# Kernel tuning notes

Hardware: AMD Instinct MI355X
Metric: run time of the kernel (lower is better)

Reference implementation:

```python
import jax, jax.numpy as jnp
import numpy as np

B, C, T = 32, 32, 1024
K = 64          # kernel_size
DIL = 1         # dilation
MLP_DIM = 256
HID = 256       # mlp_hidden_dim; TanhBlock dims: 256 -> 256 -> 128 -> 1
NF = min(MLP_DIM, K // 2 + 1)          # 33 rfft bins kept
FFT_DIM = C * NF * 2                   # 2112
N_WIN = T - DIL * (K - 1)              # 961 windows


def setup_inputs() -> dict:
    key = jax.random.key(0)
    ks = jax.random.split(key, 8)
    s = 0.02
    return {
        "x": jax.random.normal(ks[0], (B, C, T), dtype=jnp.float32),
        "Wp": jax.random.normal(ks[1], (MLP_DIM, FFT_DIM), dtype=jnp.float32) * s,
        "bp": jnp.zeros((MLP_DIM,), dtype=jnp.float32),
        "W1": jax.random.normal(ks[2], (HID, MLP_DIM), dtype=jnp.float32) * s,
        "b1": jnp.zeros((HID,), dtype=jnp.float32),
        "W2": jax.random.normal(ks[3], (HID // 2, HID), dtype=jnp.float32) * s,
        "b2": jnp.zeros((HID // 2,), dtype=jnp.float32),
        "Wout": jax.random.normal(ks[4], (1, HID // 2), dtype=jnp.float32) * s,
        "bout": jnp.zeros((1,), dtype=jnp.float32),
        "agg": jnp.zeros((N_WIN,), dtype=jnp.float32),
    }


def reference(x, Wp, bp, W1, b1, W2, b2, Wout, bout, agg):
    # Gather all dilated windows at once: window t uses indices (t-start)+k*DIL.
    base = jnp.arange(N_WIN)[:, None] + jnp.arange(K)[None, :] * DIL  # [W, K]
    win = x[:, :, base]                          # [B, C, W, K]
    fft = jnp.fft.rfft(win, axis=-1)[..., :NF]   # [B, C, W, NF] complex
    mag = jnp.log1p(jnp.abs(fft))
    ph = jnp.angle(fft) / np.pi
    feat = jnp.stack([mag, ph], axis=-1)         # [B, C, W, NF, 2]
    # torch reshape order is (C, NF, 2) -> move window axis before channel
    feat = feat.transpose(0, 2, 1, 3, 4).reshape(B, N_WIN, FFT_DIM)  # [B, W, FFT_DIM]
    proj = jnp.tanh(feat @ Wp.T + bp) * np.pi    # [B, W, MLP_DIM]
    h = jnp.tanh(proj @ W1.T + b1)               # [B, W, HID]
    h = jnp.tanh(h @ W2.T + b2)                  # [B, W, HID//2]
    out = (h @ Wout.T + bout)[..., 0]            # [B, W]
    wts = jax.nn.softmax(agg)                    # [W]
    return (out * wts[None, :]).sum(axis=1)      # [B]
```

## Files before the change

### kernel.cpp

```cpp
#include <hip/hip_runtime.h>
#include <math.h>

#define B_   32
#define C_   32
#define T_   1024
#define NF_  33
#define F2_  66
#define FD_  2112
#define NW_  961
#define MLP_ 256
#define HID_ 256
#define HH_  128
#define TN_  32
#define NT_  31

#define PI_F     3.14159265358979323846f
#define LN2_F    0.69314718055994530942f
#define L2E2_F   2.88539008177792681472f

typedef unsigned short u16;
typedef unsigned int   u32;
typedef __attribute__((ext_vector_type(8))) short bf16x8;
typedef __attribute__((ext_vector_type(4))) float f32x4;

__device__ __forceinline__ u16 f2bf(float f) {
    u32 u = __float_as_uint(f);
    u = u + 0x7FFFu + ((u >> 16) & 1u);
    return (u16)(u >> 16);
}
__device__ __forceinline__ float bf2f(u16 h) {
    return __uint_as_float((u32)h << 16);
}
__device__ __forceinline__ u32 pk_bf16(float lo, float hi) {
    u32 r;
    asm("v_cvt_pk_bf16_f32 %0, %1, %2" : "=v"(r) : "v"(lo), "v"(hi));
    return r;
}
__device__ __forceinline__ void gload16(const void* g, void* l) {
    __builtin_amdgcn_global_load_lds(
        (const __attribute__((address_space(1))) void*)g,
        (__attribute__((address_space(3))) void*)l, 16, 0, 0);
}
__device__ __forceinline__ float ftanh(float x) {
    float z = __builtin_amdgcn_exp2f(x * L2E2_F);
    return 1.f - 2.f * __builtin_amdgcn_rcpf(z + 1.f);
}
__device__ __forceinline__ float flog1p(float x) {
    return __builtin_amdgcn_logf(1.f + x) * LN2_F;
}
__device__ __forceinline__ float fatan2pi(float y, float x) {
    const float ay = fabsf(y), ax = fabsf(x);
    const float mn = fminf(ay, ax), mx = fmaxf(ay, ax);
    float t = mn * __builtin_amdgcn_rcpf(mx);
    t = (mx == 0.f) ? 0.f : t;
    const float s = t * t;
    float p = -0.00373098f;
    p = fmaf(p, s,  0.01676008f);
    p = fmaf(p, s, -0.03706162f);
    p = fmaf(p, s,  0.06160679f);
    p = fmaf(p, s, -0.10587735f);
    p = fmaf(p, s,  0.31830265f);
    p *= t;
    p = (ay > ax) ? 0.5f - p : p;
    p = (x < 0.f) ? 1.0f - p : p;
    return copysignf(p, y);
}

__global__ __launch_bounds__(256) void prep_kernel(
        const float* __restrict__ Wp, const float* __restrict__ W1,
        const float* __restrict__ W2, const float* __restrict__ agg,
        u16* __restrict__ WpH, u16* __restrict__ W1H, u16* __restrict__ W2H,
        float* __restrict__ wts) {
    const int blk = blockIdx.x;
    const int tid = threadIdx.x;
    if (blk < 128) {
        const int total = MLP_ * FD_;
        for (int i = blk * 256 + tid; i < total; i += 128 * 256)
            WpH[i] = f2bf(Wp[i]);
    } else if (blk < 160) {
        const int total = HID_ * MLP_;
        for (int i = (blk - 128) * 256 + tid; i < total; i += 32 * 256)
            W1H[i] = f2bf(W1[i]);
    } else if (blk < 176) {
        const int total = HH_ * HID_;
        for (int i = (blk - 160) * 256 + tid; i < total; i += 16 * 256)
            W2H[i] = f2bf(W2[i]);
    } else {
        __shared__ float red[256];
        float mx = -INFINITY;
        for (int i = tid; i < NW_; i += 256) mx = fmaxf(mx, agg[i]);
        red[tid] = mx; __syncthreads();
        for (int s = 128; s > 0; s >>= 1) {
            if (tid < s) red[tid] = fmaxf(red[tid], red[tid + s]);
            __syncthreads();
        }
        mx = red[0]; __syncthreads();
        float sm = 0.f;
        for (int i = tid; i < NW_; i += 256) sm += expf(agg[i] - mx);
        red[tid] = sm; __syncthreads();
        for (int s = 128; s > 0; s >>= 1) {
            if (tid < s) red[tid] += red[tid + s];
            __syncthreads();
        }
        const float inv = 1.f / red[0];
        for (int i = tid; i < NW_; i += 256) wts[i] = expf(agg[i] - mx) * inv;
    }
}

__global__ __launch_bounds__(256) void feat_kernel(const float* __restrict__ x,
                                                   u32* __restrict__ featP) {
    const int n0 = blockIdx.x * TN_;
    const int cg = blockIdx.y;
    const int bb = blockIdx.z;
    const int tid = threadIdx.x;
    const int tf = tid & 31;
    const int c8 = tid >> 5;
    const int c  = cg * 8 + c8;

    __shared__ float2 stab[64];
    __shared__ float xs[8][96];
    __shared__ float basisT[64][68];

    if (tid < 64) {
        float s, cc;
        sincosf(-PI_F * (float)tid / 32.0f, &s, &cc);
        stab[tid] = make_float2(cc, s);
    }
    __syncthreads();
    for (int e = tid; e < 2048; e += 256) {
        const int f = e >> 6, k = e & 63;
        const float2 w = stab[(f * k) & 63];
        basisT[k][2 * f]     = w.x;
        basisT[k][2 * f + 1] = w.y;
    }
    if (tid < 192) {
        const int cs = tid / 24, q = tid % 24;
        const int t0 = n0 + q * 4;
        const float* xb = x + ((size_t)bb * C_ + cg * 8 + cs) * T_;
        float4 v;
        if (t0 + 3 < T_) {
            v = *(const float4*)(xb + t0);
        } else {
            v.x = (t0 + 0 < T_) ? xb[t0 + 0] : 0.f;
            v.y = (t0 + 1 < T_) ? xb[t0 + 1] : 0.f;
            v.z = (t0 + 2 < T_) ? xb[t0 + 2] : 0.f;
            v.w = 0.f;
        }
        *(float4*)&xs[cs][q * 4] = v;
    }
    __syncthreads();

    const size_t rowb = (size_t)bb * NW_;

    {
        float re = 0.f, im = 0.f;
#pragma unroll
        for (int k = 0; k < 64; ++k) {
            const float xv = xs[c8][k];
            const float2 w = *(const float2*)&basisT[k][2 * tf];
            re = fmaf(xv, w.x, re);
            im = fmaf(xv, w.y, im);
        }
        const float2 st = stab[tf];
        const float cx = st.x, sx = -st.y;

        u32* fp = featP + (rowb + n0) * (FD_ / 2) + 33 * c + tf;
        const int nw = (NW_ - n0 < TN_) ? (NW_ - n0) : TN_;
        for (int j = 0; j < nw; ++j) {
            const float r   = __builtin_amdgcn_sqrtf(fmaf(re, re, im * im));
            const float mag = flog1p(r);
            const float ph  = fatan2pi(im, re);
            *fp = pk_bf16(mag, ph);
            fp += FD_ / 2;
            const float tre = re - xs[c8][j] + xs[c8][j + 64];
            re = tre * cx - im * sx;
            im = tre * sx + im * cx;
        }
    }

    {
        const int j   = tid & 31;
        const int c8n = tid >> 5;
        const int gn  = n0 + j;
        if (gn < NW_) {
            float s = 0.f;
#pragma unroll
            for (int k = 0; k < 32; ++k)
                s += xs[c8n][j + 2 * k] - xs[c8n][j + 2 * k + 1];
            const float a = flog1p(fabsf(s));
            const float p = (__float_as_uint(s) >> 31) ? 1.0f : 0.0f;
            featP[(rowb + gn) * (FD_ / 2) + 33 * (cg * 8 + c8n) + 32] =
                pk_bf16(a, p);
        }
    }
}

__global__ __launch_bounds__(512, 2) void gemm1t_kernel(
        const u16* __restrict__ A, const u16* __restrict__ BH,
        const float* __restrict__ bias, float scale,
        u16* __restrict__ outH, int Mvalid, int Kd) {
    constexpr int STEPB = 8192 + 16384;
    __shared__ char lds[3 * STEPB];

    const int bm = blockIdx.x;
    const int tid = threadIdx.x;
    const int lane = tid & 63, w = tid >> 6;
    const int wr = w >> 2, wc = w & 3;
    const int m0 = bm * 128;

    f32x4 acc[4][4];
#pragma unroll
    for (int i = 0; i < 4; ++i)
#pragma unroll
        for (int j = 0; j < 4; ++j) acc[i][j] = (f32x4){0.f, 0.f, 0.f, 0.f};

    const size_t rs = (size_t)Kd * 2;
    const char* gA = (const char*)A + (size_t)m0 * rs;
    const char* gB = (const char*)BH;

    auto st1 = [&](const char* g, char* l, int idx) {
        const int row = idx >> 2;
        const int kc  = (idx & 3) ^ ((row >> 1) & 3);
        gload16(g + (size_t)row * rs + (size_t)(kc << 4), l + idx * 16);
    };
    auto stage = [&](int buf, int t) {
        const size_t k0b = (size_t)t << 6;
        char* lb = lds + buf * STEPB;
        st1(gA + k0b, lb, tid);
        st1(gB + k0b, lb + 8192, tid);
        st1(gB + k0b, lb + 8192, tid + 512);
    };

    const int ra_ = wr * 64 + (lane & 15);
    const int rb_ = wc * 64 + (lane & 15);
    const int q   = lane >> 4;
    const int abase = ra_ * 64 + ((q ^ ((ra_ >> 1) & 3)) << 4);
    const int bbase = rb_ * 64 + ((q ^ ((rb_ >> 1) & 3)) << 4);

    const int nt = Kd >> 5;

    stage(0, 0);
    stage(1, 1);

    int cur = 0;
    for (int t = 0; t < nt; ++t) {
        if (t + 1 < nt)
            asm volatile("s_waitcnt vmcnt(3)" ::: "memory");
        else
            asm volatile("s_waitcnt vmcnt(0)" ::: "memory");
        __builtin_amdgcn_sched_barrier(0);
        __builtin_amdgcn_s_barrier();
        asm volatile("" ::: "memory");

        int pf = cur + 2; if (pf >= 3) pf -= 3;
        if (t + 2 < nt) stage(pf, t + 2);

        const char* lb = lds + cur * STEPB;
        bf16x8 a4[4], b4[4];
#pragma unroll
        for (int f = 0; f < 4; ++f) {
            a4[f] = *(const bf16x8*)(lb + abase + f * 1024);
            b4[f] = *(const bf16x8*)(lb + 8192 + bbase + f * 1024);
        }
        __builtin_amdgcn_s_setprio(1);
#pragma unroll
        for (int fm = 0; fm < 4; ++fm)
#pragma unroll
            for (int fn = 0; fn < 4; ++fn)
                acc[fm][fn] = __builtin_amdgcn_mfma_f32_16x16x32_bf16(a4[fm], b4[fn], acc[fm][fn], 0, 0, 0);
        __builtin_amdgcn_s_setprio(0);
        ++cur; if (cur >= 3) cur -= 3;
    }

    float bv[4];
#pragma unroll
    for (int fn = 0; fn < 4; ++fn) bv[fn] = bias[wc * 64 + fn * 16 + (lane & 15)];
#pragma unroll
    for (int fm = 0; fm < 4; ++fm) {
        const int rbase = m0 + wr * 64 + fm * 16 + (lane >> 4) * 4;
#pragma unroll
        for (int fn = 0; fn < 4; ++fn) {
            const int col = wc * 64 + fn * 16 + (lane & 15);
#pragma unroll
            for (int r = 0; r < 4; ++r) {
                const int row = rbase + r;
                if (row < Mvalid) {
                    const float v = ftanh(acc[fm][fn][r] + bv[fn]) * scale;
                    outH[(size_t)row * 256 + col] = f2bf(v);
                }
            }
        }
    }
}

__global__ __launch_bounds__(512, 1) void mlp_tail_kernel(
        const u16* __restrict__ A, const u16* __restrict__ W1Hp,
        const float* __restrict__ b1, const u16* __restrict__ W2Hp,
        const float* __restrict__ b2, const float* __restrict__ Wout,
        const float* __restrict__ bout, const float* __restrict__ wts,
        float* __restrict__ partial, int Mvalid) {
    constexpr int STEPB = 8192 + 16384;
    constexpr int OFFX  = 3 * STEPB;
    __shared__ char lds[OFFX + 65536];

    const int bm = blockIdx.x;
    const int tid = threadIdx.x;
    const int lane = tid & 63, w = tid >> 6;
    const int m0 = bm * 128;
    const size_t rs = 512;

    {
        const int wr = w >> 2, wc = w & 3;
        f32x4 acc[4][4];
#pragma unroll
        for (int i = 0; i < 4; ++i)
#pragma unroll
            for (int j = 0; j < 4; ++j) acc[i][j] = (f32x4){0.f, 0.f, 0.f, 0.f};

        const char* gA = (const char*)A + (size_t)m0 * rs;
        const char* gB = (const char*)W1Hp;

        auto st1 = [&](const char* g, char* l, int idx) {
            const int row = idx >> 2;
            const int kc  = (idx & 3) ^ ((row >> 1) & 3);
            gload16(g + (size_t)row * rs + (size_t)(kc << 4), l + idx * 16);
        };
        auto stage = [&](int buf, int t) {
            const size_t k0b = (size_t)t << 6;
            char* lb = lds + buf * STEPB;
            st1(gA + k0b, lb, tid);
            st1(gB + k0b, lb + 8192, tid);
            st1(gB + k0b, lb + 8192, tid + 512);
        };

        const int ra_ = wr * 64 + (lane & 15);
        const int rb_ = wc * 64 + (lane & 15);
        const int q   = lane >> 4;
        const int abase = ra_ * 64 + ((q ^ ((ra_ >> 1) & 3)) << 4);
        const int bbase = rb_ * 64 + ((q ^ ((rb_ >> 1) & 3)) << 4);

        stage(0, 0);
        stage(1, 1);

        int cur = 0;
        for (int t = 0; t < 8; ++t) {
            if (t + 1 < 8)
                asm volatile("s_waitcnt vmcnt(3)" ::: "memory");
            else
                asm volatile("s_waitcnt vmcnt(0)" ::: "memory");
            __builtin_amdgcn_sched_barrier(0);
            __builtin_amdgcn_s_barrier();
            asm volatile("" ::: "memory");

            int pf = cur + 2; if (pf >= 3) pf -= 3;
            if (t + 2 < 8) stage(pf, t + 2);

            const char* lb = lds + cur * STEPB;
            bf16x8 a4[4], b4[4];
#pragma unroll
            for (int f = 0; f < 4; ++f) {
                a4[f] = *(const bf16x8*)(lb + abase + f * 1024);
                b4[f] = *(const bf16x8*)(lb + 8192 + bbase + f * 1024);
            }
            __builtin_amdgcn_s_setprio(1);
#pragma unroll
            for (int fm = 0; fm < 4; ++fm)
#pragma unroll
                for (int fn = 0; fn < 4; ++fn)
                    acc[fm][fn] = __builtin_amdgcn_mfma_f32_16x16x32_bf16(a4[fm], b4[fn], acc[fm][fn], 0, 0, 0);
            __builtin_amdgcn_s_setprio(0);
            ++cur; if (cur >= 3) cur -= 3;
        }

        float bv[4];
#pragma unroll
        for (int fn = 0; fn < 4; ++fn) bv[fn] = b1[wc * 64 + fn * 16 + (lane & 15)];
#pragma unroll
        for (int fm = 0; fm < 4; ++fm) {
#pragma unroll
            for (int fn = 0; fn < 4; ++fn) {
                const int col = wc * 64 + fn * 16 + (lane & 15);
                const int cpart = ((col >> 5) << 6) + ((col & 7) * 2);
                const int kc = (col >> 3) & 3;
#pragma unroll
                for (int r = 0; r < 4; ++r) {
                    const int row = wr * 64 + fm * 16 + (lane >> 4) * 4 + r;
                    const float v = ftanh(acc[fm][fn][r] + bv[fn]);
                    const int byt = row * 512 + cpart + ((kc ^ ((row >> 1) & 3)) << 4);
                    *(u16*)(lds + OFFX + byt) = f2bf(v);
                }
            }
        }
    }
    __syncthreads();

    f32x4 acc2[4][4];
#pragma unroll
    for (int i = 0; i < 4; ++i)
#pragma unroll
        for (int j = 0; j < 4; ++j) acc2[i][j] = (f32x4){0.f, 0.f, 0.f, 0.f};

    const int wr2 = (w >> 1) & 1, wc2 = w & 1;
    {
        const char* gB2 = (const char*)W2Hp;
        auto st2 = [&](int buf, int t) {
            const size_t k0b = (size_t)t << 6;
            const int row = tid >> 2;
            const int kc  = (tid & 3) ^ ((row >> 1) & 3);
            gload16(gB2 + (size_t)row * rs + k0b + (size_t)(kc << 4),
                    lds + buf * STEPB + tid * 16);
        };
        st2(0, 0);
        st2(1, 1);

        const int q = lane >> 4;
        const int rb = wc2 * 64 + (lane & 15);
        const int bbase = rb * 64 + ((q ^ ((rb >> 1) & 3)) << 4);
        const int ra = wr2 * 64 + (lane & 15);
        const int abase = ra * 512 + ((q ^ ((ra >> 1) & 3)) << 4);

        int cur = 0;
        for (int t = 0; t < 8; ++t) {
            if (t + 1 < 8)
                asm volatile("s_waitcnt vmcnt(1)" ::: "memory");
            else
                asm volatile("s_waitcnt vmcnt(0)" ::: "memory");
            __builtin_amdgcn_sched_barrier(0);
            __builtin_amdgcn_s_barrier();
            asm volatile("" ::: "memory");

            int pf = cur + 2; if (pf >= 3) pf -= 3;
            if (t + 2 < 8) st2(pf, t + 2);

            if (w < 4) {
                const char* lb = lds + cur * STEPB;
                bf16x8 a4[4], b4[4];
#pragma unroll
                for (int f = 0; f < 4; ++f) {
                    a4[f] = *(const bf16x8*)(lds + OFFX + abase + f * 8192 + t * 64);
                    b4[f] = *(const bf16x8*)(lb + bbase + f * 1024);
                }
                __builtin_amdgcn_s_setprio(1);
#pragma unroll
                for (int fm = 0; fm < 4; ++fm)
#pragma unroll
                    for (int fn = 0; fn < 4; ++fn)
                        acc2[fm][fn] = __builtin_amdgcn_mfma_f32_16x16x32_bf16(a4[fm], b4[fn], acc2[fm][fn], 0, 0, 0);
                __builtin_amdgcn_s_setprio(0);
            }
            ++cur; if (cur >= 3) cur -= 3;
        }
    }

    __syncthreads();
    float* rsum = (float*)lds;
    float* red  = (float*)(lds + 1024);

    if (w < 4) {
        float bv[4], wv[4];
#pragma unroll
        for (int fn = 0; fn < 4; ++fn) {
            const int col = wc2 * 64 + fn * 16 + (lane & 15);
            bv[fn] = b2[col];
            wv[fn] = Wout[col];
        }
#pragma unroll
        for (int fm = 0; fm < 4; ++fm) {
#pragma unroll
            for (int r = 0; r < 4; ++r) {
                float c = 0.f;
#pragma unroll
                for (int fn = 0; fn < 4; ++fn)
                    c += ftanh(acc2[fm][fn][r] + bv[fn]) * wv[fn];
                c += __shfl_xor(c, 1);
                c += __shfl_xor(c, 2);
                c += __shfl_xor(c, 4);
                c += __shfl_xor(c, 8);
                if ((lane & 15) == 0)
                    rsum[(wr2 * 64 + fm * 16 + (lane >> 4) * 4 + r) * 2 + wc2] = c;
            }
        }
    }
    __syncthreads();

    const float bO = bout[0];
    float val = 0.f;
    int rowb = -1;
    if (tid < 128) {
        const int gr = m0 + tid;
        if (gr < Mvalid) {
            const float dot = rsum[tid * 2] + rsum[tid * 2 + 1] + bO;
            rowb = gr / NW_;
            val = dot * wts[gr - rowb * NW_];
        }
    }
    __syncthreads();

    const int bFirst = m0 / NW_;
    if (tid < 256) red[tid] = (tid < 128 && rowb == bFirst) ? val : 0.f;
    __syncthreads();
    for (int s = 128; s > 0; s >>= 1) {
        if (tid < s) red[tid] += red[tid + s];
        __syncthreads();
    }
    if (tid == 0) partial[bm * 2] = red[0];
    __syncthreads();
    if (tid < 256) red[tid] = (tid < 128 && rowb == bFirst + 1) ? val : 0.f;
    __syncthreads();
    for (int s = 128; s > 0; s >>= 1) {
        if (tid < s) red[tid] += red[tid + s];
        __syncthreads();
    }
    if (tid == 0) partial[bm * 2 + 1] = red[0];
}

__global__ __launch_bounds__(64) void finred_kernel(const float* __restrict__ partial,
                                                    float* __restrict__ out,
                                                    int nbat, int nblocks) {
    const int b = threadIdx.x;
    if (b >= nbat) return;
    int lo = (b * NW_) / 128;
    int hi = ((b + 1) * NW_ - 1) / 128;
    if (hi > nblocks - 1) hi = nblocks - 1;
    float s = 0.f;
    for (int bm = lo; bm <= hi; ++bm) {
        const int slot = ((bm * 128) / NW_ == b) ? 0 : 1;
        s += partial[bm * 2 + slot];
    }
    out[b] = s;
}

extern "C" void kernel_launch(void* const* d_in, const int* in_sizes, int n_in,
                              void* d_out, int out_size, void* d_ws, size_t ws_size,
                              hipStream_t stream) {
    const float* x    = (const float*)d_in[0];
    const float* Wp   = (const float*)d_in[1];
    const float* bp   = (const float*)d_in[2];
    const float* W1   = (const float*)d_in[3];
    const float* b1   = (const float*)d_in[4];
    const float* W2   = (const float*)d_in[5];
    const float* b2   = (const float*)d_in[6];
    const float* Wout = (const float*)d_in[7];
    const float* bout = (const float*)d_in[8];
    const float* agg  = (const float*)d_in[9];
    float* out = (float*)d_out;

    char* wsb = (char*)d_ws;
    size_t off = 0;
    auto ra = [](size_t b) { return (b + 255) & ~(size_t)255; };
    auto alloc = [&](size_t bytes) -> char* {
        char* p = wsb + off;
        off += ra(bytes);
        return p;
    };

    u16* WpH = (u16*)alloc((size_t)MLP_ * FD_ * 2);
    u16* W1H = (u16*)alloc((size_t)HID_ * MLP_ * 2);
    u16* W2H = (u16*)alloc((size_t)HH_ * HID_ * 2);
    float* wts = (float*)alloc((size_t)NW_ * 4);

    const size_t fixed = off;
    int NB = 32;
    for (;;) {
        const size_t M = (size_t)NB * NW_;
        const size_t Mp = ((M + 127) / 128) * 128;
        const size_t need = ra(Mp * FD_ * 2) +
                            ra(Mp * 256 * 2) +
                            ra((Mp / 128) * 2 * 4);
        if (fixed + need <= ws_size || NB == 1) break;
        NB >>= 1;
    }
    const size_t Mmax  = (size_t)NB * NW_;
    const size_t MpMax = ((Mmax + 127) / 128) * 128;
    u16* featH = (u16*)alloc(MpMax * FD_ * 2);
    u16* projH = (u16*)alloc(MpMax * 256 * 2);
    float* partial = (float*)alloc((MpMax / 128) * 2 * 4);

    prep_kernel<<<dim3(177), dim3(256), 0, stream>>>(
        Wp, W1, W2, agg, WpH, W1H, W2H, wts);

    for (int b0 = 0; b0 < B_; b0 += NB) {
        const int nb = (B_ - b0 < NB) ? (B_ - b0) : NB;
        const int M = nb * NW_;
        const int Mp = ((M + 127) / 128) * 128;

        feat_kernel<<<dim3(NT_, 4, nb), dim3(256), 0, stream>>>(
            x + (size_t)b0 * C_ * T_, (u32*)featH);

        gemm1t_kernel<<<dim3(Mp / 128), dim3(512), 0, stream>>>(
            featH, WpH, bp, PI_F, projH, M, FD_);

        mlp_tail_kernel<<<dim3(Mp / 128), dim3(512), 0, stream>>>(
            projH, W1H, b1, W2H, b2, Wout, bout, wts, partial, M);

        finred_kernel<<<dim3(1), dim3(64), 0, stream>>>(
            partial, out + b0, nb, Mp / 128);
    }
}
```

Baseline: 124.5 us.

## Double GEMM K-step to 64 and shorten atan2 polynomial

The projection GEMM now stages 64-wide K slices per pipeline step, doubling the LDS tile. It widens the XOR swizzle to 8 chunks and issues two MFMA passes per barrier, which halves the number of loop iterations and synchronizations. Launch bounds drop to one block per CU because of the larger LDS footprint, trading occupancy for fewer barriers. The phase atan2 approximation also uses a lower-degree polynomial, which cuts ALU work in the feature kernel at some cost in accuracy.

Measured after the change: 119.3 us. 1.04x faster.

```diff
diff --git a/kernel.cpp b/kernel.cpp
--- a/kernel.cpp
+++ b/kernel.cpp
@@ -54,12 +54,10 @@
     float t = mn * __builtin_amdgcn_rcpf(mx);
     t = (mx == 0.f) ? 0.f : t;
     const float s = t * t;
-    float p = -0.00373098f;
-    p = fmaf(p, s,  0.01676008f);
-    p = fmaf(p, s, -0.03706162f);
-    p = fmaf(p, s,  0.06160679f);
-    p = fmaf(p, s, -0.10587735f);
-    p = fmaf(p, s,  0.31830265f);
+    float p = -0.027097f;
+    p = fmaf(p, s,  0.057337f);
+    p = fmaf(p, s, -0.105130f);
+    p = fmaf(p, s,  0.318268f);
     p *= t;
     p = (ay > ax) ? 0.5f - p : p;
     p = (x < 0.f) ? 1.0f - p : p;
@@ -195,11 +193,11 @@
     }
 }
 
-__global__ __launch_bounds__(512, 2) void gemm1t_kernel(
+__global__ __launch_bounds__(512, 1) void gemm64_kernel(
         const u16* __restrict__ A, const u16* __restrict__ BH,
         const float* __restrict__ bias, float scale,
         u16* __restrict__ outH, int Mvalid, int Kd) {
-    constexpr int STEPB = 8192 + 16384;
+    constexpr int STEPB = 16384 + 32768;
     __shared__ char lds[3 * STEPB];
 
     const int bm = blockIdx.x;
@@ -219,25 +217,32 @@
     const char* gB = (const char*)BH;
 
     auto st1 = [&](const char* g, char* l, int idx) {
-        const int row = idx >> 2;
-        const int kc  = (idx & 3) ^ ((row >> 1) & 3);
+        const int row = idx >> 3;
+        const int kc  = (idx & 7) ^ ((row >> 1) & 7);
         gload16(g + (size_t)row * rs + (size_t)(kc << 4), l + idx * 16);
     };
     auto stage = [&](int buf, int t) {
-        const size_t k0b = (size_t)t << 6;
+        const size_t k0b = (size_t)t << 7;
         char* lb = lds + buf * STEPB;
         st1(gA + k0b, lb, tid);
-        st1(gB + k0b, lb + 8192, tid);
-        st1(gB + k0b, lb + 8192, tid + 512);
+        st1(gA + k0b, lb, tid + 512);
+        st1(gB + k0b, lb + 16384, tid);
+        st1(gB + k0b, lb + 16384, tid + 512);
+        st1(gB + k0b, lb + 16384, tid + 1024);
+        st1(gB + k0b, lb + 16384, tid + 1536);
     };
 
+    const int q   = lane >> 4;
     const int ra_ = wr * 64 + (lane & 15);
     const int rb_ = wc * 64 + (lane & 15);
-    const int q   = lane >> 4;
-    const int abase = ra_ * 64 + ((q ^ ((ra_ >> 1) & 3)) << 4);
-    const int bbase = rb_ * 64 + ((q ^ ((rb_ >> 1) & 3)) << 4);
-
-    const int nt = Kd >> 5;
+    const int s3a = (ra_ >> 1) & 7;
+    const int s3b = (rb_ >> 1) & 7;
+    const int ab0 = ra_ * 128 + (((0 * 4 + q) ^ s3a) << 4);
+    const int ab1 = ra_ * 128 + (((1 * 4 + q) ^ s3a) << 4);
+    const int bb0 = rb_ * 128 + (((0 * 4 + q) ^ s3b) << 4);
+    const int bb1 = rb_ * 128 + (((1 * 4 + q) ^ s3b) << 4);
+
+    const int nt = Kd >> 6;
 
     stage(0, 0);
     stage(1, 1);
@@ -245,7 +250,7 @@
     int cur = 0;
     for (int t = 0; t < nt; ++t) {
         if (t + 1 < nt)
-            asm volatile("s_waitcnt vmcnt(3)" ::: "memory");
+            asm volatile("s_waitcnt vmcnt(6)" ::: "memory");
         else
             asm volatile("s_waitcnt vmcnt(0)" ::: "memory");
         __builtin_amdgcn_sched_barrier(0);
@@ -256,18 +261,25 @@
         if (t + 2 < nt) stage(pf, t + 2);
 
         const char* lb = lds + cur * STEPB;
-        bf16x8 a4[4], b4[4];
+        bf16x8 a0[4], a1[4], b0[4], b1[4];
 #pragma unroll
         for (int f = 0; f < 4; ++f) {
-            a4[f] = *(const bf16x8*)(lb + abase + f * 1024);
-            b4[f] = *(const bf16x8*)(lb + 8192 + bbase + f * 1024);
+            a0[f] = *(const bf16x8*)(lb + ab0 + f * 2048);
+            a1[f] = *(const bf16x8*)(lb + ab1 + f * 2048);
+            b0[f] = *(const bf16x8*)(lb + 16384 + bb0 + f * 2048);
+            b1[f] = *(const bf16x8*)(lb + 16384 + bb1 + f * 2048);
         }
         __builtin_amdgcn_s_setprio(1);
 #pragma unroll
         for (int fm = 0; fm < 4; ++fm)
 #pragma unroll
             for (int fn = 0; fn < 4; ++fn)
-                acc[fm][fn] = __builtin_amdgcn_mfma_f32_16x16x32_bf16(a4[fm], b4[fn], acc[fm][fn], 0, 0, 0);
+                acc[fm][fn] = __builtin_amdgcn_mfma_f32_16x16x32_bf16(a0[fm], b0[fn], acc[fm][fn], 0, 0, 0);
+#pragma unroll
+        for (int fm = 0; fm < 4; ++fm)
+#pragma unroll
+            for (int fn = 0; fn < 4; ++fn)
+                acc[fm][fn] = __builtin_amdgcn_mfma_f32_16x16x32_bf16(a1[fm], b1[fn], acc[fm][fn], 0, 0, 0);
         __builtin_amdgcn_s_setprio(0);
         ++cur; if (cur >= 3) cur -= 3;
     }
@@ -587,7 +599,7 @@
         feat_kernel<<<dim3(NT_, 4, nb), dim3(256), 0, stream>>>(
             x + (size_t)b0 * C_ * T_, (u32*)featH);
 
-        gemm1t_kernel<<<dim3(Mp / 128), dim3(512), 0, stream>>>(
+        gemm64_kernel<<<dim3(Mp / 128), dim3(512), 0, stream>>>(
             featH, WpH, bp, PI_F, projH, M, FD_);
 
         mlp_tail_kernel<<<dim3(Mp / 128), dim3(512), 0, stream>>>(
```
